# Kernel tuning notes

Hardware: AMD Instinct MI355X
Metric: run time of the kernel (lower is better)

The kernel has to match this reference:

```python
import jax, jax.numpy as jnp
import numpy as np

N = 4096       # num nodes == output_dim (delta is symmetrized NxN)
E = 65536      # num edges (avg degree 16)
IN_DIM = 128
H = 256        # hidden_dim (channels)
HEADS = 4


def setup_inputs():
    key = jax.random.key(0)
    ks = iter(jax.random.split(key, 40))
    def w(shape, s=0.05):
        return jax.random.normal(next(ks), shape, jnp.float32) * s
    inp = {}
    inp['x'] = jax.random.normal(next(ks), (N, IN_DIM), jnp.float32)
    inp['edge_index'] = jax.random.randint(next(ks), (2, E), 0, N)
    inp['pre_w'] = w((H, IN_DIM)); inp['pre_b'] = w((H,))
    for p in ('g1', 'g2'):
        inp[p + '_gcn_w'] = w((H, H)); inp[p + '_gcn_b'] = w((H,))
        inp[p + '_attn_in_w'] = w((3 * H, H)); inp[p + '_attn_in_b'] = w((3 * H,))
        inp[p + '_attn_out_w'] = w((H, H)); inp[p + '_attn_out_b'] = w((H,))
        inp[p + '_ffn_w1'] = w((2 * H, H)); inp[p + '_ffn_b1'] = w((2 * H,))
        inp[p + '_ffn_w2'] = w((H, 2 * H)); inp[p + '_ffn_b2'] = w((H,))
    inp['mlp_w1'] = w((H, H)); inp['mlp_b1'] = w((H,))
    inp['mlp_w2'] = w((N, H)); inp['mlp_b2'] = w((N,))
    return inp


def _gcn(x, src, dst, W, b):
    n = x.shape[0]
    x = x @ W.T
    loop = jnp.arange(n)
    s = jnp.concatenate([src, loop])
    d = jnp.concatenate([dst, loop])
    deg = jax.ops.segment_sum(jnp.ones(s.shape[0], x.dtype), d, num_segments=n)
    dinv = jnp.where(deg > 0, jax.lax.rsqrt(deg), 0.0)
    coef = (dinv[s] * dinv[d])[:, None]
    out = jax.ops.segment_sum(x[s] * coef, d, num_segments=n)
    return out + b


def _mha(h, in_w, in_b, out_w, out_b):
    # nn.MultiheadAttention self-attention over all N nodes (single dense graph)
    n, c = h.shape
    d = c // HEADS
    qkv = h @ in_w.T + in_b                      # [N, 3C]
    q, k, v = jnp.split(qkv, 3, axis=-1)
    q = q.reshape(n, HEADS, d).transpose(1, 0, 2) * (d ** -0.5)  # [h, n, d]
    k = k.reshape(n, HEADS, d).transpose(1, 0, 2)
    v = v.reshape(n, HEADS, d).transpose(1, 0, 2)
    a = jax.nn.softmax(jnp.einsum('hnd,hmd->hnm', q, k), axis=-1)
    o = jnp.einsum('hnm,hmd->hnd', a, v).transpose(1, 0, 2).reshape(n, c)
    return o @ out_w.T + out_b


def _gps(x, src, dst, gw, gb, iw, ib, ow, ob, w1, b1, w2, b2):
    # GPSConv, eval mode: dropout off, batch_norm (default running stats) = identity
    h1 = _gcn(x, src, dst, gw, gb) + x
    h2 = _mha(x, iw, ib, ow, ob) + x
    out = h1 + h2
    ff = jax.nn.relu(out @ w1.T + b1) @ w2.T + b2
    return out + ff


def reference(x, edge_index, pre_w, pre_b,
              g1_gcn_w, g1_gcn_b, g1_attn_in_w, g1_attn_in_b, g1_attn_out_w, g1_attn_out_b,
              g1_ffn_w1, g1_ffn_b1, g1_ffn_w2, g1_ffn_b2,
              g2_gcn_w, g2_gcn_b, g2_attn_in_w, g2_attn_in_b, g2_attn_out_w, g2_attn_out_b,
              g2_ffn_w1, g2_ffn_b1, g2_ffn_w2, g2_ffn_b2,
              mlp_w1, mlp_b1, mlp_w2, mlp_b2):
    src, dst = edge_index[0], edge_index[1]
    h = jax.nn.relu(x @ pre_w.T + pre_b)
    h = jax.nn.relu(_gps(h, src, dst, g1_gcn_w, g1_gcn_b, g1_attn_in_w, g1_attn_in_b,
                         g1_attn_out_w, g1_attn_out_b, g1_ffn_w1, g1_ffn_b1, g1_ffn_w2, g1_ffn_b2))
    h = jax.nn.relu(_gps(h, src, dst, g2_gcn_w, g2_gcn_b, g2_attn_in_w, g2_attn_in_b,
                         g2_attn_out_w, g2_attn_out_b, g2_ffn_w1, g2_ffn_b1, g2_ffn_w2, g2_ffn_b2))
    delta = jax.nn.relu(h @ mlp_w1.T + mlp_b1) @ mlp_w2.T + mlp_b2  # [N, N]
    return (delta + delta.T) * 0.5
```

## Files before the change

### kernel.cpp

```cpp
#include <hip/hip_runtime.h>

#define NN 4096
#define EE 65536
#define HC 256

typedef unsigned short ushort_t;
typedef __attribute__((ext_vector_type(8))) short bf16x8;
typedef __attribute__((ext_vector_type(4))) float f32x4;

__device__ __forceinline__ ushort_t f2bf(float f) {
    unsigned int u = __float_as_uint(f);
    unsigned int r = (u + 0x7fffu + ((u >> 16) & 1u)) >> 16;
    return (ushort_t)r;
}
__device__ __forceinline__ float bf2f(ushort_t u) {
    return __uint_as_float(((unsigned int)u) << 16);
}
__device__ __forceinline__ unsigned int pack2bf(float a, float b) {
    unsigned int ua = __float_as_uint(a) + 0x8000u;
    unsigned int ub = __float_as_uint(b) + 0x8000u;
    return __builtin_amdgcn_perm(ub, ua, 0x07060302u);
}

__global__ void deg_init_k(float* __restrict__ deg) {
    int i = blockIdx.x * 256 + threadIdx.x;
    deg[i] = 1.0f;
}
__global__ void deg_scatter_k(const int* __restrict__ dst, float* __restrict__ deg) {
    int e = blockIdx.x * 256 + threadIdx.x;
    atomicAdd(&deg[dst[e]], 1.0f);
}
__global__ void dinv_k(const float* __restrict__ deg, float* __restrict__ dinv) {
    int i = blockIdx.x * 256 + threadIdx.x;
    dinv[i] = rsqrtf(deg[i]);
}
__global__ __launch_bounds__(1024)
void scan_offsets_k(const float* __restrict__ deg, int* __restrict__ offs,
                    int* __restrict__ cursor) {
    __shared__ int part[1024];
    const int t = threadIdx.x;
    int c0 = (int)deg[t * 4 + 0] - 1;
    int c1 = (int)deg[t * 4 + 1] - 1;
    int c2 = (int)deg[t * 4 + 2] - 1;
    int c3 = (int)deg[t * 4 + 3] - 1;
    part[t] = c0 + c1 + c2 + c3;
    __syncthreads();
    for (int off = 1; off < 1024; off <<= 1) {
        int v = (t >= off) ? part[t - off] : 0;
        __syncthreads();
        part[t] += v;
        __syncthreads();
    }
    int base = (t == 0) ? 0 : part[t - 1];
    offs[t * 4 + 0] = base;
    offs[t * 4 + 1] = base + c0;
    offs[t * 4 + 2] = base + c0 + c1;
    offs[t * 4 + 3] = base + c0 + c1 + c2;
    cursor[t * 4 + 0] = base;
    cursor[t * 4 + 1] = base + c0;
    cursor[t * 4 + 2] = base + c0 + c1;
    cursor[t * 4 + 3] = base + c0 + c1 + c2;
    if (t == 1023) offs[4096] = part[1023];
}
__global__ void csr_fill_k(const int* __restrict__ src, const int* __restrict__ dst,
                           int* __restrict__ cursor, int* __restrict__ csr_src) {
    int e = blockIdx.x * 256 + threadIdx.x;
    int pos = atomicAdd(&cursor[dst[e]], 1);
    csr_src[pos] = src[e];
}

__global__ __launch_bounds__(256)
void gcn_gather_k(const float* __restrict__ xw, const float* __restrict__ dinv,
                  const int* __restrict__ offs, const int* __restrict__ csr_src,
                  float* __restrict__ agg) {
    const int node = blockIdx.x * 4 + (threadIdx.x >> 6);
    const int c = (threadIdx.x & 63) * 4;
    const float dd = dinv[node];
    float4 a = *(const float4*)&xw[(size_t)node * HC + c];
    const float self = dd * dd;
    float4 acc = make_float4(a.x * self, a.y * self, a.z * self, a.w * self);
    const int beg = offs[node], end = offs[node + 1];
    for (int e = beg; e < end; e++) {
        int s = csr_src[e];
        float coef = dinv[s] * dd;
        const float4 v = *(const float4*)&xw[(size_t)s * HC + c];
        acc.x += v.x * coef;
        acc.y += v.y * coef;
        acc.z += v.z * coef;
        acc.w += v.w * coef;
    }
    *(float4*)&agg[(size_t)node * HC + c] = acc;
}

__global__ void cvt_bf16_k(const float* __restrict__ in, ushort_t* __restrict__ out) {
    int i = (blockIdx.x * 256 + threadIdx.x) * 4;
    float4 v = *(const float4*)&in[i];
    unsigned int d0 = pack2bf(v.x, v.y), d1 = pack2bf(v.z, v.w);
    *(uint2*)&out[i] = make_uint2(d0, d1);
}

__global__ __launch_bounds__(256)
void gemm_bf_k(const float* __restrict__ X, const float* __restrict__ W,
               const float* __restrict__ bias1, const float* __restrict__ bias2,
               const float* __restrict__ res1, const float* __restrict__ res2, float res2scale,
               float* __restrict__ out, int K, int M, int dorelu, int obf,
               int colsplit, const float* __restrict__ W2,
               const float* __restrict__ bias_r2, float* __restrict__ out2, int M2)
{
    __shared__ ushort_t As[64][72];
    __shared__ ushort_t Bs[32][72];
    const int t = threadIdx.x;
    const int w = t >> 6, lane = t & 63;
    const int m = lane & 15, quad = lane >> 4;
    const int row0 = blockIdx.y << 6, col0 = blockIdx.x << 5;
    const int sr = t >> 2;
    const int sc = (t & 3) << 4;
    const int wr2 = t >> 3;
    const int wc2 = (t & 7) << 3;

    const float* Wu = W;
    const float* b1u = bias1;
    const float* b2u = bias2;
    float* outu = out;
    int Mu = M, colu = col0;
    if (colsplit > 0 && col0 >= colsplit) {
        Wu = W2; b1u = bias_r2; b2u = nullptr;
        outu = out2; Mu = M2; colu = col0 - colsplit;
    }

    f32x4 acc[2] = {};
    for (int k0 = 0; k0 < K; k0 += 64) {
        const float* xp = &X[(size_t)(row0 + sr) * K + k0 + sc];
        const float* wp = &Wu[(size_t)(colu + wr2) * K + k0 + wc2];
        float4 xa = *(const float4*)xp,       xb = *(const float4*)(xp + 4);
        float4 xc = *(const float4*)(xp + 8), xd = *(const float4*)(xp + 12);
        float4 wa = *(const float4*)wp,       wb = *(const float4*)(wp + 4);
        __syncthreads();
        {
            unsigned int tx[8];
            tx[0] = pack2bf(xa.x, xa.y); tx[1] = pack2bf(xa.z, xa.w);
            tx[2] = pack2bf(xb.x, xb.y); tx[3] = pack2bf(xb.z, xb.w);
            tx[4] = pack2bf(xc.x, xc.y); tx[5] = pack2bf(xc.z, xc.w);
            tx[6] = pack2bf(xd.x, xd.y); tx[7] = pack2bf(xd.z, xd.w);
            *(uint4*)&As[sr][sc]     = *(const uint4*)&tx[0];
            *(uint4*)&As[sr][sc + 8] = *(const uint4*)&tx[4];
            unsigned int tw[4];
            tw[0] = pack2bf(wa.x, wa.y); tw[1] = pack2bf(wa.z, wa.w);
            tw[2] = pack2bf(wb.x, wb.y); tw[3] = pack2bf(wb.z, wb.w);
            *(uint4*)&Bs[wr2][wc2] = *(const uint4*)&tw[0];
        }
        __syncthreads();
        #pragma unroll
        for (int kc = 0; kc < 2; kc++) {
            bf16x8 af = *(const bf16x8*)&As[(w << 4) + m][kc * 32 + quad * 8];
            #pragma unroll
            for (int cb = 0; cb < 2; cb++) {
                bf16x8 bf = *(const bf16x8*)&Bs[cb * 16 + m][kc * 32 + quad * 8];
                acc[cb] = __builtin_amdgcn_mfma_f32_16x16x32_bf16(af, bf, acc[cb], 0, 0, 0);
            }
        }
    }
    #pragma unroll
    for (int cb = 0; cb < 2; cb++) {
        #pragma unroll
        for (int r = 0; r < 4; r++) {
            const int row = row0 + (w << 4) + quad * 4 + r;
            const int col = colu + cb * 16 + m;
            float v = acc[cb][r];
            if (b1u) v += b1u[col];
            if (b2u) v += b2u[col];
            if (res1) v += res1[(size_t)row * Mu + col];
            if (res2) v += res2scale * res2[(size_t)row * Mu + col];
            if (dorelu) v = fmaxf(v, 0.f);
            if (obf) ((ushort_t*)outu)[(size_t)row * Mu + col] = f2bf(v);
            else outu[(size_t)row * Mu + col] = v;
        }
    }
}

__global__ __launch_bounds__(256)
void kv_prep_k(const float* __restrict__ qkv, ushort_t* __restrict__ Kb,
               ushort_t* __restrict__ Vtb)
{
    __shared__ ushort_t Vs[64][72];
    const int h = blockIdx.y;
    const int n0 = blockIdx.x << 6;
    const int t = threadIdx.x;
    for (int u = t; u < 1024; u += 256) {
        int r = u >> 4, c = u & 15;
        const float* kp = &qkv[(size_t)(n0 + r) * 768 + 256 + h * 64 + c * 4];
        float4 kv = *(const float4*)kp;
        float4 vv = *(const float4*)(kp + 256);
        *(uint2*)&Kb[((size_t)(h * 4096 + n0 + r)) * 64 + c * 4] =
            make_uint2(pack2bf(kv.x, kv.y), pack2bf(kv.z, kv.w));
        *(uint2*)&Vs[r][c * 4] =
            make_uint2(pack2bf(vv.x, vv.y), pack2bf(vv.z, vv.w));
    }
    __syncthreads();
    int d = t >> 2, kc = t & 3;
    __attribute__((aligned(16))) ushort_t vals[16];
    #pragma unroll
    for (int k = 0; k < 16; k++) vals[k] = Vs[kc * 16 + k][d];
    ushort_t* op = &Vtb[((size_t)(h * 64 + d)) * 4096 + n0 + kc * 16];
    *(uint4*)op = *(const uint4*)&vals[0];
    *(uint4*)(op + 8) = *(const uint4*)&vals[8];
}

__global__ __launch_bounds__(256)
void attn_part_k(const float* qkv, const ushort_t* __restrict__ Kb,
                 const ushort_t* __restrict__ Vtb, ushort_t* opart,
                 float* __restrict__ m_part, float* __restrict__ l_part)
{
    __shared__ ushort_t Kt[64][72];
    __shared__ ushort_t Vt[64][72];
    __shared__ ushort_t Plb[4][16][72];
    const int h = blockIdx.y & 3;
    const int split = blockIdx.y >> 2;
    const int q0 = blockIdx.x << 6;
    const int t = threadIdx.x;
    const int w = t >> 6, lane = t & 63;
    const int m = lane & 15, quad = lane >> 4;

    const float qs = 0.125f * 1.44269504f;
    bf16x8 qf[2];
    #pragma unroll
    for (int kc = 0; kc < 2; kc++) {
        const float* qp = &qkv[(size_t)(q0 + w * 16 + m) * 768 + h * 64 + kc * 32 + quad * 8];
        float4 a = *(const float4*)qp;
        float4 b = *(const float4*)(qp + 4);
        qf[kc][0] = (short)f2bf(a.x * qs);
        qf[kc][1] = (short)f2bf(a.y * qs);
        qf[kc][2] = (short)f2bf(a.z * qs);
        qf[kc][3] = (short)f2bf(a.w * qs);
        qf[kc][4] = (short)f2bf(b.x * qs);
        qf[kc][5] = (short)f2bf(b.y * qs);
        qf[kc][6] = (short)f2bf(b.z * qs);
        qf[kc][7] = (short)f2bf(b.w * qs);
    }
    bf16x8 onesf;
    #pragma unroll
    for (int j = 0; j < 8; j++) onesf[j] = (short)0x3F80;

    f32x4 o[4], ol;
    float mrow[4];
    #pragma unroll
    for (int i = 0; i < 4; i++) {
        o[i] = (f32x4){0.f, 0.f, 0.f, 0.f};
        mrow[i] = -1e30f;
    }
    ol = (f32x4){0.f, 0.f, 0.f, 0.f};

    for (int kb = split * 16; kb < split * 16 + 16; kb++) {
        __syncthreads();
        for (int u = t; u < 512; u += 256) {
            int r = u >> 3, c = u & 7;
            int pr = ((r & 15) << 2) | (r >> 4);
            *(uint4*)&Kt[r][c * 8] = *(const uint4*)&Kb[((size_t)(h * 4096 + kb * 64 + pr)) * 64 + c * 8];
            *(uint4*)&Vt[r][c * 8] = *(const uint4*)&Vtb[((size_t)(h * 64 + r)) * 4096 + kb * 64 + c * 8];
        }
        __syncthreads();

        f32x4 s[4];
        #pragma unroll
        for (int b = 0; b < 4; b++) s[b] = (f32x4){0.f, 0.f, 0.f, 0.f};
        #pragma unroll
        for (int b = 0; b < 4; b++)
            #pragma unroll
            for (int kc = 0; kc < 2; kc++) {
                bf16x8 kf = *(const bf16x8*)&Kt[b * 16 + m][kc * 32 + quad * 8];
                s[b] = __builtin_amdgcn_mfma_f32_16x16x32_bf16(qf[kc], kf, s[b], 0, 0, 0);
            }

        #pragma unroll
        for (int r = 0; r < 4; r++) {
            float mx = fmaxf(fmaxf(s[0][r], s[1][r]), fmaxf(s[2][r], s[3][r]));
            #pragma unroll
            for (int off = 1; off < 16; off <<= 1)
                mx = fmaxf(mx, __shfl_xor(mx, off));
            float mn = fmaxf(mrow[r], mx);
            float alpha = __builtin_amdgcn_exp2f(mrow[r] - mn);
            mrow[r] = mn;
            unsigned int d0 = pack2bf(__builtin_amdgcn_exp2f(s[0][r] - mn),
                                      __builtin_amdgcn_exp2f(s[1][r] - mn));
            unsigned int d1 = pack2bf(__builtin_amdgcn_exp2f(s[2][r] - mn),
                                      __builtin_amdgcn_exp2f(s[3][r] - mn));
            *(uint2*)&Plb[w][quad * 4 + r][m * 4] = make_uint2(d0, d1);
            o[0][r] *= alpha; o[1][r] *= alpha;
            o[2][r] *= alpha; o[3][r] *= alpha;
            ol[r] *= alpha;
        }

        #pragma unroll
        for (int kc = 0; kc < 2; kc++) {
            bf16x8 pa = *(const bf16x8*)&Plb[w][m][kc * 32 + quad * 8];
            #pragma unroll
            for (int nb = 0; nb < 4; nb++) {
                bf16x8 vf = *(const bf16x8*)&Vt[nb * 16 + m][kc * 32 + quad * 8];
                o[nb] = __builtin_amdgcn_mfma_f32_16x16x32_bf16(pa, vf, o[nb], 0, 0, 0);
            }
            ol = __builtin_amdgcn_mfma_f32_16x16x32_bf16(pa, onesf, ol, 0, 0, 0);
        }
    }

    #pragma unroll
    for (int nb = 0; nb < 4; nb++)
        #pragma unroll
        for (int r = 0; r < 4; r++) {
            int q = q0 + w * 16 + quad * 4 + r;
            opart[(size_t)q * 1536 + 512 + split * 256 + h * 64 + nb * 16 + m] = f2bf(o[nb][r]);
        }
    if (m == 0) {
        #pragma unroll
        for (int r = 0; r < 4; r++) {
            int q = q0 + w * 16 + quad * 4 + r;
            m_part[(split * 4 + h) * 4096 + q] = mrow[r];
            l_part[(split * 4 + h) * 4096 + q] = ol[r];
        }
    }
}

__global__ __launch_bounds__(256)
void attn_merge_k(const ushort_t* __restrict__ opart, const float* __restrict__ m_part,
                  const float* __restrict__ l_part, float* __restrict__ att)
{
    int idx = blockIdx.x * 256 + threadIdx.x;
    int q = idx >> 8, c = idx & 255;
    int h = c >> 6, d = c & 63;
    float ms[4];
    float mmax = -1e30f;
    #pragma unroll
    for (int s = 0; s < 4; s++) {
        ms[s] = m_part[(s * 4 + h) * 4096 + q];
        mmax = fmaxf(mmax, ms[s]);
    }
    float onum = 0.f, lden = 0.f;
    #pragma unroll
    for (int s = 0; s < 4; s++) {
        float wgt = __builtin_amdgcn_exp2f(ms[s] - mmax);
        float ov = bf2f(opart[(size_t)q * 1536 + 512 + s * 256 + h * 64 + d]);
        onum += wgt * ov;
        lden += wgt * l_part[(s * 4 + h) * 4096 + q];
    }
    att[(size_t)q * 256 + c] = onum / lden;
}

__global__ __launch_bounds__(256)
void sym_mlp_mfma_k(const ushort_t* __restrict__ Tb, const ushort_t* __restrict__ Wb,
                    const float* __restrict__ b2, float* __restrict__ out)
{
    __shared__ ushort_t As[128][72];
    __shared__ ushort_t Bs[128][72];
    const int t = threadIdx.x;
    const int w = t >> 6, lane = t & 63;
    const int m = lane & 15, quad = lane >> 4;
    const int wr = (w >> 1) * 64, wc = (w & 1) * 64;
    const int ri = blockIdx.y * 128, rj = blockIdx.x * 128;

    f32x4 acc[4][4] = {};
    for (int kk = 0; kk < 8; kk++) {
        const int k0 = kk * 64;
        const ushort_t* Asrc = (k0 < 256) ? Tb : Wb;
        const ushort_t* Bsrc = (k0 < 256) ? Wb : Tb;
        const int kcol = k0 & 255;
        __syncthreads();
        #pragma unroll
        for (int i = 0; i < 4; i++) {
            int s = t + i * 256;
            int row = s >> 3, ch = (s & 7) * 8;
            *(uint4*)&As[row][ch] = *(const uint4*)&Asrc[(size_t)(ri + row) * 256 + kcol + ch];
            *(uint4*)&Bs[row][ch] = *(const uint4*)&Bsrc[(size_t)(rj + row) * 256 + kcol + ch];
        }
        __syncthreads();
        #pragma unroll
        for (int kc = 0; kc < 2; kc++) {
            bf16x8 af[4], bfr[4];
            #pragma unroll
            for (int rb = 0; rb < 4; rb++)
                af[rb] = *(const bf16x8*)&As[wr + rb * 16 + m][kc * 32 + quad * 8];
            #pragma unroll
            for (int cb = 0; cb < 4; cb++)
                bfr[cb] = *(const bf16x8*)&Bs[wc + cb * 16 + m][kc * 32 + quad * 8];
            #pragma unroll
            for (int rb = 0; rb < 4; rb++)
                #pragma unroll
                for (int cb = 0; cb < 4; cb++)
                    acc[rb][cb] = __builtin_amdgcn_mfma_f32_16x16x32_bf16(af[rb], bfr[cb], acc[rb][cb], 0, 0, 0);
        }
    }
    #pragma unroll
    for (int rb = 0; rb < 4; rb++) {
        #pragma unroll
        for (int r = 0; r < 4; r++) {
            const int gr = ri + wr + rb * 16 + quad * 4 + r;
            const float br = b2[gr];
            #pragma unroll
            for (int cb = 0; cb < 4; cb++) {
                const int gc = rj + wc + cb * 16 + m;
                out[(size_t)gr * NN + gc] = 0.5f * (acc[rb][cb][r] + br + b2[gc]);
            }
        }
    }
}

extern "C" void kernel_launch(void* const* d_in, const int* in_sizes, int n_in,
                              void* d_out, int out_size, void* d_ws, size_t ws_size,
                              hipStream_t stream) {
    (void)in_sizes; (void)n_in; (void)out_size; (void)ws_size;
    const float* x = (const float*)d_in[0];
    const int* ei = (const int*)d_in[1];
    const int* src = ei;
    const int* dst = ei + EE;

    float* ws = (float*)d_ws;
    const int NH = NN * HC;
    float* h0  = ws;
    float* hb  = ws + 1 * NH;
    float* hc  = ws + 2 * NH;
    float* att = ws + 3 * NH;
    float* qkv = ws + 4 * NH;
    float* ffh = ws + 4 * NH;
    float* deg = ws + 7 * NH;
    float* dinv = deg + NN;
    int* offs    = (int*)(dinv + NN);
    int* cursor  = offs + 4100;
    int* csr_src = cursor + 4096;
    float* m_part = (float*)(csr_src + EE);
    float* l_part = m_part + 65536;
    ushort_t* Kb  = (ushort_t*)hc;
    ushort_t* Vtb = Kb + NH;
    ushort_t* Tb  = (ushort_t*)hb;
    ushort_t* W2b = Tb + NH;

    deg_init_k<<<NN / 256, 256, 0, stream>>>(deg);
    deg_scatter_k<<<EE / 256, 256, 0, stream>>>(dst, deg);
    dinv_k<<<NN / 256, 256, 0, stream>>>(deg, dinv);
    scan_offsets_k<<<1, 1024, 0, stream>>>(deg, offs, cursor);
    csr_fill_k<<<EE / 256, 256, 0, stream>>>(src, dst, cursor, csr_src);

    gemm_bf_k<<<dim3(8, 64), 256, 0, stream>>>(
        x, (const float*)d_in[2], (const float*)d_in[3], nullptr,
        nullptr, nullptr, 0.f, h0, 128, 256, 1, 0,
        0, nullptr, nullptr, nullptr, 0);

    for (int L = 0; L < 2; L++) {
        int B = 4 + L * 10;
        const float* gw = (const float*)d_in[B + 0];
        const float* gb = (const float*)d_in[B + 1];
        const float* iw = (const float*)d_in[B + 2];
        const float* ib = (const float*)d_in[B + 3];
        const float* ow = (const float*)d_in[B + 4];
        const float* ob = (const float*)d_in[B + 5];
        const float* w1 = (const float*)d_in[B + 6];
        const float* b1 = (const float*)d_in[B + 7];
        const float* w2 = (const float*)d_in[B + 8];
        const float* b2 = (const float*)d_in[B + 9];

        gemm_bf_k<<<dim3(32, 64), 256, 0, stream>>>(
            h0, gw, nullptr, nullptr, nullptr, nullptr, 0.f, att, 256, 256, 0, 0,
            256, iw, ib, qkv, 768);
        gcn_gather_k<<<NN / 4, 256, 0, stream>>>(att, dinv, offs, csr_src, hb);
        kv_prep_k<<<dim3(64, 4), 256, 0, stream>>>(qkv, Kb, Vtb);
        attn_part_k<<<dim3(64, 16), 256, 0, stream>>>(
            qkv, Kb, Vtb, (ushort_t*)qkv, m_part, l_part);
        attn_merge_k<<<NN, 256, 0, stream>>>(
            (const ushort_t*)qkv, m_part, l_part, att);
        gemm_bf_k<<<dim3(8, 64), 256, 0, stream>>>(
            att, ow, ob, gb, hb, h0, 2.0f, hc, 256, 256, 0, 0,
            0, nullptr, nullptr, nullptr, 0);
        gemm_bf_k<<<dim3(16, 64), 256, 0, stream>>>(
            hc, w1, b1, nullptr, nullptr, nullptr, 0.f, ffh, 256, 512, 1, 0,
            0, nullptr, nullptr, nullptr, 0);
        gemm_bf_k<<<dim3(8, 64), 256, 0, stream>>>(
            ffh, w2, b2, nullptr, hc, nullptr, 0.f, h0, 512, 256, 1, 0,
            0, nullptr, nullptr, nullptr, 0);
    }

    gemm_bf_k<<<dim3(8, 64), 256, 0, stream>>>(
        h0, (const float*)d_in[24], (const float*)d_in[25], nullptr,
        nullptr, nullptr, 0.f, (float*)Tb, 256, 256, 1, 1,
        0, nullptr, nullptr, nullptr, 0);
    cvt_bf16_k<<<NH / 1024, 256, 0, stream>>>((const float*)d_in[26], W2b);
    sym_mlp_mfma_k<<<dim3(32, 32), 256, 0, stream>>>(
        Tb, W2b, (const float*)d_in[27], (float*)d_out);
}
```

Baseline: 443.4 us.

## Prefetch K/V tiles into registers and skip rescale with lazy max update

```diff
diff --git a/kernel.cpp b/kernel.cpp
--- a/kernel.cpp
+++ b/kernel.cpp
@@ -221,6 +221,19 @@
     const int w = t >> 6, lane = t & 63;
     const int m = lane & 15, quad = lane >> 4;
 
+    const int r0 = t >> 3, c8 = (t & 7) << 3;
+    const int r1 = r0 + 32;
+    const int pr0 = ((r0 & 15) << 2) | (r0 >> 4);
+    const int pr1 = ((r1 & 15) << 2) | (r1 >> 4);
+    const ushort_t* kb_p0 = &Kb[((size_t)(h * 4096 + split * 1024 + pr0)) * 64 + c8];
+    const ushort_t* kb_p1 = &Kb[((size_t)(h * 4096 + split * 1024 + pr1)) * 64 + c8];
+    const ushort_t* vt_p0 = &Vtb[((size_t)(h * 64 + r0)) * 4096 + split * 1024 + c8];
+    const ushort_t* vt_p1 = &Vtb[((size_t)(h * 64 + r1)) * 4096 + split * 1024 + c8];
+    ushort_t* const kt_d0 = &Kt[r0][c8];
+    ushort_t* const kt_d1 = &Kt[r1][c8];
+    ushort_t* const vt_d0 = &Vt[r0][c8];
+    ushort_t* const vt_d1 = &Vt[r1][c8];
+
     const float qs = 0.125f * 1.44269504f;
     bf16x8 qf[2];
     #pragma unroll
@@ -250,19 +263,30 @@
     }
     ol = (f32x4){0.f, 0.f, 0.f, 0.f};
 
-    for (int kb = split * 16; kb < split * 16 + 16; kb++) {
-        __syncthreads();
-        for (int u = t; u < 512; u += 256) {
-            int r = u >> 3, c = u & 7;
-            int pr = ((r & 15) << 2) | (r >> 4);
-            *(uint4*)&Kt[r][c * 8] = *(const uint4*)&Kb[((size_t)(h * 4096 + kb * 64 + pr)) * 64 + c * 8];
-            *(uint4*)&Vt[r][c * 8] = *(const uint4*)&Vtb[((size_t)(h * 64 + r)) * 4096 + kb * 64 + c * 8];
+    uint4 kr0 = *(const uint4*)kb_p0;
+    uint4 kr1 = *(const uint4*)kb_p1;
+    uint4 vr0 = *(const uint4*)vt_p0;
+    uint4 vr1 = *(const uint4*)vt_p1;
+
+    for (int it = 0; it < 16; it++) {
+        __syncthreads();
+        *(uint4*)kt_d0 = kr0;
+        *(uint4*)kt_d1 = kr1;
+        *(uint4*)vt_d0 = vr0;
+        *(uint4*)vt_d1 = vr1;
+        if (it < 15) {
+            kb_p0 += 4096; kb_p1 += 4096; vt_p0 += 64; vt_p1 += 64;
+            kr0 = *(const uint4*)kb_p0;
+            kr1 = *(const uint4*)kb_p1;
+            vr0 = *(const uint4*)vt_p0;
+            vr1 = *(const uint4*)vt_p1;
         }
         __syncthreads();
 
         f32x4 s[4];
         #pragma unroll
         for (int b = 0; b < 4; b++) s[b] = (f32x4){0.f, 0.f, 0.f, 0.f};
+        __builtin_amdgcn_s_setprio(1);
         #pragma unroll
         for (int b = 0; b < 4; b++)
             #pragma unroll
@@ -270,26 +294,40 @@
                 bf16x8 kf = *(const bf16x8*)&Kt[b * 16 + m][kc * 32 + quad * 8];
                 s[b] = __builtin_amdgcn_mfma_f32_16x16x32_bf16(qf[kc], kf, s[b], 0, 0, 0);
             }
-
+        __builtin_amdgcn_s_setprio(0);
+
+        float mx[4];
         #pragma unroll
         for (int r = 0; r < 4; r++) {
-            float mx = fmaxf(fmaxf(s[0][r], s[1][r]), fmaxf(s[2][r], s[3][r]));
+            float v = fmaxf(fmaxf(s[0][r], s[1][r]), fmaxf(s[2][r], s[3][r]));
             #pragma unroll
             for (int off = 1; off < 16; off <<= 1)
-                mx = fmaxf(mx, __shfl_xor(mx, off));
-            float mn = fmaxf(mrow[r], mx);
-            float alpha = __builtin_amdgcn_exp2f(mrow[r] - mn);
-            mrow[r] = mn;
-            unsigned int d0 = pack2bf(__builtin_amdgcn_exp2f(s[0][r] - mn),
-                                      __builtin_amdgcn_exp2f(s[1][r] - mn));
-            unsigned int d1 = pack2bf(__builtin_amdgcn_exp2f(s[2][r] - mn),
-                                      __builtin_amdgcn_exp2f(s[3][r] - mn));
+                v = fmaxf(v, __shfl_xor(v, off));
+            mx[r] = v;
+        }
+        bool grow = (mx[0] > mrow[0] + 8.f) | (mx[1] > mrow[1] + 8.f) |
+                    (mx[2] > mrow[2] + 8.f) | (mx[3] > mrow[3] + 8.f);
+        if (__any(grow)) {
+            #pragma unroll
+            for (int r = 0; r < 4; r++) {
+                float mn = fmaxf(mrow[r], mx[r]);
+                float alpha = __builtin_amdgcn_exp2f(mrow[r] - mn);
+                mrow[r] = mn;
+                o[0][r] *= alpha; o[1][r] *= alpha;
+                o[2][r] *= alpha; o[3][r] *= alpha;
+                ol[r] *= alpha;
+            }
+        }
+        #pragma unroll
+        for (int r = 0; r < 4; r++) {
+            unsigned int d0 = pack2bf(__builtin_amdgcn_exp2f(s[0][r] - mrow[r]),
+                                      __builtin_amdgcn_exp2f(s[1][r] - mrow[r]));
+            unsigned int d1 = pack2bf(__builtin_amdgcn_exp2f(s[2][r] - mrow[r]),
+                                      __builtin_amdgcn_exp2f(s[3][r] - mrow[r]));
             *(uint2*)&Plb[w][quad * 4 + r][m * 4] = make_uint2(d0, d1);
-            o[0][r] *= alpha; o[1][r] *= alpha;
-            o[2][r] *= alpha; o[3][r] *= alpha;
-            ol[r] *= alpha;
-        }
-
+        }
+
+        __builtin_amdgcn_s_setprio(1);
         #pragma unroll
         for (int kc = 0; kc < 2; kc++) {
             bf16x8 pa = *(const bf16x8*)&Plb[w][m][kc * 32 + quad * 8];
@@ -300,6 +338,7 @@
             }
             ol = __builtin_amdgcn_mfma_f32_16x16x32_bf16(pa, onesf, ol, 0, 0, 0);
         }
+        __builtin_amdgcn_s_setprio(0);
     }
 
     #pragma unroll
```

Result: no change. 445.7 us (+0.5%).

## Rewrite attention partial kernel with 32x32 MFMA, register-resident P and lazy rescale

Applied to the files above, without the earlier changes.

```diff
diff --git a/kernel.cpp b/kernel.cpp
--- a/kernel.cpp
+++ b/kernel.cpp
@@ -7,6 +7,7 @@
 typedef unsigned short ushort_t;
 typedef __attribute__((ext_vector_type(8))) short bf16x8;
 typedef __attribute__((ext_vector_type(4))) float f32x4;
+typedef __attribute__((ext_vector_type(16))) float f32x16;
 
 __device__ __forceinline__ ushort_t f2bf(float f) {
     unsigned int u = __float_as_uint(f);
@@ -206,116 +207,163 @@
     *(uint4*)(op + 8) = *(const uint4*)&vals[8];
 }
 
-__global__ __launch_bounds__(256)
+__global__ __launch_bounds__(128)
 void attn_part_k(const float* qkv, const ushort_t* __restrict__ Kb,
                  const ushort_t* __restrict__ Vtb, ushort_t* opart,
                  float* __restrict__ m_part, float* __restrict__ l_part)
 {
-    __shared__ ushort_t Kt[64][72];
-    __shared__ ushort_t Vt[64][72];
-    __shared__ ushort_t Plb[4][16][72];
+    __shared__ ushort_t Kt[64][64];
+    __shared__ ushort_t Vt[64][64];
     const int h = blockIdx.y & 3;
     const int split = blockIdx.y >> 2;
     const int q0 = blockIdx.x << 6;
     const int t = threadIdx.x;
-    const int w = t >> 6, lane = t & 63;
-    const int m = lane & 15, quad = lane >> 4;
+    const int w = t >> 6;
+    const int lane = t & 63;
+    const int l31 = lane & 31;
+    const int hi = lane >> 5;
+
+    const int sr = t >> 3;
+    const int sc = t & 7;
+    const int swz = ((sc ^ (sr & 7)) << 3);
+    const ushort_t* kp = &Kb[((size_t)(h * 4096 + split * 1024 + sr)) * 64 + sc * 8];
+    const ushort_t* vp = &Vtb[((size_t)(h * 64 + sr)) * 4096 + split * 1024 + sc * 8];
 
     const float qs = 0.125f * 1.44269504f;
-    bf16x8 qf[2];
-    #pragma unroll
-    for (int kc = 0; kc < 2; kc++) {
-        const float* qp = &qkv[(size_t)(q0 + w * 16 + m) * 768 + h * 64 + kc * 32 + quad * 8];
+    const int qrow = q0 + w * 32 + l31;
+    bf16x8 qf[4];
+    #pragma unroll
+    for (int s = 0; s < 4; s++) {
+        const float* qp = &qkv[(size_t)qrow * 768 + h * 64 + s * 16 + hi * 8];
         float4 a = *(const float4*)qp;
         float4 b = *(const float4*)(qp + 4);
-        qf[kc][0] = (short)f2bf(a.x * qs);
-        qf[kc][1] = (short)f2bf(a.y * qs);
-        qf[kc][2] = (short)f2bf(a.z * qs);
-        qf[kc][3] = (short)f2bf(a.w * qs);
-        qf[kc][4] = (short)f2bf(b.x * qs);
-        qf[kc][5] = (short)f2bf(b.y * qs);
-        qf[kc][6] = (short)f2bf(b.z * qs);
-        qf[kc][7] = (short)f2bf(b.w * qs);
-    }
-    bf16x8 onesf;
-    #pragma unroll
-    for (int j = 0; j < 8; j++) onesf[j] = (short)0x3F80;
-
-    f32x4 o[4], ol;
-    float mrow[4];
-    #pragma unroll
-    for (int i = 0; i < 4; i++) {
-        o[i] = (f32x4){0.f, 0.f, 0.f, 0.f};
-        mrow[i] = -1e30f;
-    }
-    ol = (f32x4){0.f, 0.f, 0.f, 0.f};
-
-    for (int kb = split * 16; kb < split * 16 + 16; kb++) {
-        __syncthreads();
-        for (int u = t; u < 512; u += 256) {
-            int r = u >> 3, c = u & 7;
-            int pr = ((r & 15) << 2) | (r >> 4);
-            *(uint4*)&Kt[r][c * 8] = *(const uint4*)&Kb[((size_t)(h * 4096 + kb * 64 + pr)) * 64 + c * 8];
-            *(uint4*)&Vt[r][c * 8] = *(const uint4*)&Vtb[((size_t)(h * 64 + r)) * 4096 + kb * 64 + c * 8];
-        }
-        __syncthreads();
-
-        f32x4 s[4];
-        #pragma unroll
-        for (int b = 0; b < 4; b++) s[b] = (f32x4){0.f, 0.f, 0.f, 0.f};
-        #pragma unroll
-        for (int b = 0; b < 4; b++)
-            #pragma unroll
-            for (int kc = 0; kc < 2; kc++) {
-                bf16x8 kf = *(const bf16x8*)&Kt[b * 16 + m][kc * 32 + quad * 8];
-                s[b] = __builtin_amdgcn_mfma_f32_16x16x32_bf16(qf[kc], kf, s[b], 0, 0, 0);
+        union { uint4 u; bf16x8 v; } cv;
+        cv.u = make_uint4(pack2bf(a.x * qs, a.y * qs), pack2bf(a.z * qs, a.w * qs),
+                          pack2bf(b.x * qs, b.y * qs), pack2bf(b.z * qs, b.w * qs));
+        qf[s] = cv.v;
+    }
+
+    f32x16 O0 = {}, O1 = {};
+    float mrow = -1e30f;
+    float ol = 0.f;
+
+    for (int it = 0; it < 16; it++) {
+        uint4 k0 = *(const uint4*)kp;
+        uint4 k1 = *(const uint4*)(kp + 16 * 64);
+        uint4 k2 = *(const uint4*)(kp + 32 * 64);
+        uint4 k3 = *(const uint4*)(kp + 48 * 64);
+        uint4 v0 = *(const uint4*)vp;
+        uint4 v1 = *(const uint4*)(vp + (size_t)16 * 4096);
+        uint4 v2 = *(const uint4*)(vp + (size_t)32 * 4096);
+        uint4 v3 = *(const uint4*)(vp + (size_t)48 * 4096);
+        kp += 4096; vp += 64;
+        __syncthreads();
+        *(uint4*)&Kt[sr][swz]      = k0;
+        *(uint4*)&Kt[sr + 16][swz] = k1;
+        *(uint4*)&Kt[sr + 32][swz] = k2;
+        *(uint4*)&Kt[sr + 48][swz] = k3;
+        *(uint4*)&Vt[sr][swz]      = v0;
+        *(uint4*)&Vt[sr + 16][swz] = v1;
+        *(uint4*)&Vt[sr + 32][swz] = v2;
+        *(uint4*)&Vt[sr + 48][swz] = v3;
+        __syncthreads();
+
+        f32x16 S0 = {}, S1 = {};
+        const int kcol = ((hi) ^ (l31 & 7));
+        (void)kcol;
+        __builtin_amdgcn_s_setprio(1);
+        #pragma unroll
+        for (int s = 0; s < 4; s++) {
+            const int cc = ((2 * s + hi) ^ (l31 & 7)) << 3;
+            bf16x8 kf0 = *(const bf16x8*)&Kt[l31][cc];
+            bf16x8 kf1 = *(const bf16x8*)&Kt[l31 + 32][cc];
+            S0 = __builtin_amdgcn_mfma_f32_32x32x16_bf16(kf0, qf[s], S0, 0, 0, 0);
+            S1 = __builtin_amdgcn_mfma_f32_32x32x16_bf16(kf1, qf[s], S1, 0, 0, 0);
+        }
+        __builtin_amdgcn_s_setprio(0);
+
+        float r[32];
+        #pragma unroll
+        for (int i = 0; i < 16; i++) { r[i] = S0[i]; r[16 + i] = S1[i]; }
+        #pragma unroll
+        for (int st = 16; st > 0; st >>= 1)
+            #pragma unroll
+            for (int i = 0; i < st; i++) r[i] = fmaxf(r[i], r[i + st]);
+        float mx = fmaxf(r[0], __shfl_xor(r[0], 32));
+
+        if (__any(mx > mrow + 8.f)) {
+            float mnew = fmaxf(mrow, mx);
+            float alpha = __builtin_amdgcn_exp2f(mrow - mnew);
+            mrow = mnew;
+            ol *= alpha;
+            #pragma unroll
+            for (int rg = 0; rg < 16; rg++) {
+                float ar = __shfl(alpha, (rg & 3) + 8 * (rg >> 2) + 4 * hi);
+                O0[rg] *= ar;
+                O1[rg] *= ar;
             }
-
-        #pragma unroll
-        for (int r = 0; r < 4; r++) {
-            float mx = fmaxf(fmaxf(s[0][r], s[1][r]), fmaxf(s[2][r], s[3][r]));
-            #pragma unroll
-            for (int off = 1; off < 16; off <<= 1)
-                mx = fmaxf(mx, __shfl_xor(mx, off));
-            float mn = fmaxf(mrow[r], mx);
-            float alpha = __builtin_amdgcn_exp2f(mrow[r] - mn);
-            mrow[r] = mn;
-            unsigned int d0 = pack2bf(__builtin_amdgcn_exp2f(s[0][r] - mn),
-                                      __builtin_amdgcn_exp2f(s[1][r] - mn));
-            unsigned int d1 = pack2bf(__builtin_amdgcn_exp2f(s[2][r] - mn),
-                                      __builtin_amdgcn_exp2f(s[3][r] - mn));
-            *(uint2*)&Plb[w][quad * 4 + r][m * 4] = make_uint2(d0, d1);
-            o[0][r] *= alpha; o[1][r] *= alpha;
-            o[2][r] *= alpha; o[3][r] *= alpha;
-            ol[r] *= alpha;
-        }
-
-        #pragma unroll
-        for (int kc = 0; kc < 2; kc++) {
-            bf16x8 pa = *(const bf16x8*)&Plb[w][m][kc * 32 + quad * 8];
-            #pragma unroll
-            for (int nb = 0; nb < 4; nb++) {
-                bf16x8 vf = *(const bf16x8*)&Vt[nb * 16 + m][kc * 32 + quad * 8];
-                o[nb] = __builtin_amdgcn_mfma_f32_16x16x32_bf16(pa, vf, o[nb], 0, 0, 0);
-            }
-            ol = __builtin_amdgcn_mfma_f32_16x16x32_bf16(pa, onesf, ol, 0, 0, 0);
-        }
-    }
-
-    #pragma unroll
-    for (int nb = 0; nb < 4; nb++)
-        #pragma unroll
-        for (int r = 0; r < 4; r++) {
-            int q = q0 + w * 16 + quad * 4 + r;
-            opart[(size_t)q * 1536 + 512 + split * 256 + h * 64 + nb * 16 + m] = f2bf(o[nb][r]);
-        }
-    if (m == 0) {
-        #pragma unroll
-        for (int r = 0; r < 4; r++) {
-            int q = q0 + w * 16 + quad * 4 + r;
-            m_part[(split * 4 + h) * 4096 + q] = mrow[r];
-            l_part[(split * 4 + h) * 4096 + q] = ol[r];
-        }
+        }
+
+        #pragma unroll
+        for (int i = 0; i < 16; i++) S0[i] = __builtin_amdgcn_exp2f(S0[i] - mrow);
+        #pragma unroll
+        for (int i = 0; i < 16; i++) S1[i] = __builtin_amdgcn_exp2f(S1[i] - mrow);
+
+        float a2[32];
+        #pragma unroll
+        for (int i = 0; i < 16; i++) { a2[i] = S0[i]; a2[16 + i] = S1[i]; }
+        #pragma unroll
+        for (int st = 16; st > 0; st >>= 1)
+            #pragma unroll
+            for (int i = 0; i < st; i++) a2[i] += a2[i + st];
+        ol += a2[0] + __shfl_xor(a2[0], 32);
+
+        unsigned c[16], d[16];
+        #pragma unroll
+        for (int i = 0; i < 8; i++) c[i] = pack2bf(S0[2 * i], S0[2 * i + 1]);
+        #pragma unroll
+        for (int i = 0; i < 8; i++) c[8 + i] = pack2bf(S1[2 * i], S1[2 * i + 1]);
+        #pragma unroll
+        for (int i = 0; i < 16; i++) d[i] = __shfl_xor(c[i], 32);
+
+        bf16x8 pa[4];
+        #pragma unroll
+        for (int b = 0; b < 2; b++) {
+            union { uint4 u; bf16x8 v; } t0, t1;
+            t0.u = make_uint4(hi ? d[8 * b + 2] : c[8 * b + 0],
+                              hi ? d[8 * b + 3] : c[8 * b + 1],
+                              hi ? c[8 * b + 2] : d[8 * b + 0],
+                              hi ? c[8 * b + 3] : d[8 * b + 1]);
+            t1.u = make_uint4(hi ? d[8 * b + 6] : c[8 * b + 4],
+                              hi ? d[8 * b + 7] : c[8 * b + 5],
+                              hi ? c[8 * b + 6] : d[8 * b + 4],
+                              hi ? c[8 * b + 7] : d[8 * b + 5]);
+            pa[2 * b] = t0.v;
+            pa[2 * b + 1] = t1.v;
+        }
+
+        __builtin_amdgcn_s_setprio(1);
+        #pragma unroll
+        for (int ks = 0; ks < 4; ks++) {
+            const int cc = ((2 * ks + hi) ^ (l31 & 7)) << 3;
+            bf16x8 vf0 = *(const bf16x8*)&Vt[l31][cc];
+            bf16x8 vf1 = *(const bf16x8*)&Vt[l31 + 32][cc];
+            O0 = __builtin_amdgcn_mfma_f32_32x32x16_bf16(pa[ks], vf0, O0, 0, 0, 0);
+            O1 = __builtin_amdgcn_mfma_f32_32x32x16_bf16(pa[ks], vf1, O1, 0, 0, 0);
+        }
+        __builtin_amdgcn_s_setprio(0);
+    }
+
+    #pragma unroll
+    for (int rg = 0; rg < 16; rg++) {
+        int q = q0 + w * 32 + (rg & 3) + 8 * (rg >> 2) + 4 * hi;
+        size_t base = (size_t)q * 1536 + 512 + split * 256 + h * 64;
+        opart[base + l31] = f2bf(O0[rg]);
+        opart[base + 32 + l31] = f2bf(O1[rg]);
+    }
+    if (hi == 0) {
+        m_part[(split * 4 + h) * 4096 + q0 + w * 32 + l31] = mrow;
+        l_part[(split * 4 + h) * 4096 + q0 + w * 32 + l31] = ol;
     }
 }
 
@@ -460,7 +508,7 @@
             256, iw, ib, qkv, 768);
         gcn_gather_k<<<NN / 4, 256, 0, stream>>>(att, dinv, offs, csr_src, hb);
         kv_prep_k<<<dim3(64, 4), 256, 0, stream>>>(qkv, Kb, Vtb);
-        attn_part_k<<<dim3(64, 16), 256, 0, stream>>>(
+        attn_part_k<<<dim3(64, 16), 128, 0, stream>>>(
             qkv, Kb, Vtb, (ushort_t*)qkv, m_part, l_part);
         attn_merge_k<<<NN, 256, 0, stream>>>(
             (const ushort_t*)qkv, m_part, l_part, att);
```

Result: faster. 420.0 us (-5.3%).
